# Kernel optimization log

Hardware: AMD Instinct MI355X
Metric: run time of the kernel (lower is better)

Reference implementation:

```python
import jax, jax.numpy as jnp
import numpy as np

B, S, N, D = 2048, 8, 32, 64


def setup_inputs() -> dict:
    key = jax.random.key(0)
    ks = jax.random.split(key, 13)
    s1 = 1.0 / np.sqrt(2 * D + 6)
    s2 = 1.0 / np.sqrt(D)
    s3 = 1.0 / np.sqrt(D // 2)
    return {
        "celestial_tensor": jax.random.normal(ks[0], (B, S, N, D), jnp.float32),
        "theta": jax.random.normal(ks[1], (B, N), jnp.float32),
        "phi": jax.random.normal(ks[2], (B, N), jnp.float32),
        "velocity": jax.random.normal(ks[3], (B, N), jnp.float32),
        "radius": jax.random.uniform(ks[4], (B, N), jnp.float32),
        "longitude": jax.random.normal(ks[5], (B, N), jnp.float32),
        "W1": jax.random.uniform(ks[6], (2 * D + 6, D), jnp.float32, -s1, s1),
        "b1": jax.random.uniform(ks[7], (D,), jnp.float32, -s1, s1),
        "W2": jax.random.uniform(ks[8], (D, D // 2), jnp.float32, -s2, s2),
        "b2": jax.random.uniform(ks[9], (D // 2,), jnp.float32, -s2, s2),
        "W3": jax.random.uniform(ks[10], (D // 2, 1), jnp.float32, -s3, s3),
        "b3": jax.random.uniform(ks[11], (1,), jnp.float32, -s3, s3),
        "phase_weights": jnp.ones((6,), jnp.float32),
    }


def _circ(a, b):
    # circular difference wrapped to (-pi, pi]
    d = a - b
    return jnp.arctan2(jnp.sin(d), jnp.cos(d))


def reference(celestial_tensor, theta, phi, velocity, radius, longitude,
              W1, b1, W2, b2, W3, b3, phase_weights):
    Bb, _, Nn, _ = celestial_tensor.shape
    feats = celestial_tensor[:, -1]  # [B, N, D] last timestep
    ii, jj = np.triu_indices(Nn, 1)  # static upper-tri pair indices, P pairs
    fi = feats[:, ii]  # [B, P, D]
    fj = feats[:, jj]
    td = _circ(theta[:, ii], theta[:, jj])
    pd = _circ(phi[:, ii], phi[:, jj])
    vd = velocity[:, ii] - velocity[:, jj]
    rr = radius[:, ii] / (radius[:, jj] + 1e-8)
    ld = _circ(longitude[:, ii], longitude[:, jj])
    pr = jnp.cos(td) * jnp.cos(pd)  # phase_relationship
    scal = jnp.stack([td, pd, vd, rr, ld, pr], axis=-1)  # [B, P, 6]
    x = jnp.concatenate([fi, fj, scal], axis=-1)  # [B, P, 2D+6]
    h = jax.nn.gelu(x @ W1 + b1, approximate=False)
    h = jax.nn.gelu(h @ W2 + b2, approximate=False)
    edge = jax.nn.sigmoid((h @ W3 + b3)[..., 0])  # [B, P]
    pf = jnp.stack([jnp.abs(td), jnp.abs(pd), jnp.abs(vd),
                    jnp.abs(rr - 1.0), jnp.abs(ld), jnp.abs(pr)], axis=-1)
    gate = jax.nn.sigmoid(jnp.sum(pf * phase_weights, axis=-1))
    fe = edge * gate  # [B, P]
    adj = jnp.zeros((Bb, Nn, Nn), dtype=fe.dtype)
    adj = adj.at[:, ii, jj].set(fe).at[:, jj, ii].set(fe)
    return adj
```

## Files before the change

### kernel.cpp

```cpp
#include <hip/hip_runtime.h>
#include <hip/hip_bf16.h>
#include <math.h>

#define SS 8
#define NN 32
#define DD 64
#define NP 496
#define LDA 68

typedef short v8s __attribute__((ext_vector_type(8)));
typedef float v4f __attribute__((ext_vector_type(4)));
typedef float f2  __attribute__((ext_vector_type(2)));

union FragU { uint4 u; v8s s; };
union Q2    { float4 q; f2 h[2]; };

static __device__ __forceinline__ f2 f2m(float a, float b) { f2 r; r.x = a; r.y = b; return r; }
static __device__ __forceinline__ f2 splat2(float s) { f2 r; r.x = s; r.y = s; return r; }
static __device__ __forceinline__ f2 pk_fma(f2 a, f2 b, f2 c) {
#if __has_builtin(__builtin_elementwise_fma)
    return __builtin_elementwise_fma(a, b, c);
#else
    return f2m(fmaf(a.x, b.x, c.x), fmaf(a.y, b.y, c.y));
#endif
}

__device__ __forceinline__ float wrap_pi(float d) {
    return fmaf(-6.28318530717958647692f, rintf(d * 0.15915494309189533577f), d);
}
__device__ __forceinline__ float sigmoid_(float x) {
    return __builtin_amdgcn_rcpf(1.0f + __expf(-x));
}
__device__ __forceinline__ f2 gelu2(f2 xin) {
    f2 z = xin * splat2(0.70710678118654752440f);
#if __has_builtin(__builtin_elementwise_max)
    f2 az = __builtin_elementwise_max(z, -z);
#else
    f2 az = f2m(fabsf(z.x), fabsf(z.y));
#endif
    f2 d = pk_fma(splat2(0.078108f), az, splat2(0.000972f));
    d = pk_fma(d, az, splat2(0.230389f));
    d = pk_fma(d, az, splat2(0.278393f));
    d = pk_fma(d, az, splat2(1.0f));
    f2 t = f2m(__builtin_amdgcn_rcpf(d.x), __builtin_amdgcn_rcpf(d.y));
    f2 t2 = t * t;
    f2 r = pk_fma(-t2, t2, splat2(1.0f));
    unsigned int rx = __float_as_uint(r.x) | (__float_as_uint(z.x) & 0x80000000u);
    unsigned int ry = __float_as_uint(r.y) | (__float_as_uint(z.y) & 0x80000000u);
    f2 er = f2m(__uint_as_float(rx), __uint_as_float(ry));
    return xin * pk_fma(er, splat2(0.5f), splat2(0.5f));
}
__device__ __forceinline__ unsigned int pack_bf16_rne(float x0, float x1) {
    union { __hip_bfloat162 h2; unsigned int u; } cv;
    float2 f; f.x = x0; f.y = x1;
    cv.h2 = __float22bfloat162_rn(f);
    return cv.u;
}
__device__ __forceinline__ float row_reduce16(float x) {
    int v;
    v = __builtin_amdgcn_update_dpp(0, __float_as_int(x), 0x128, 0xf, 0xf, false);
    x += __int_as_float(v);
    v = __builtin_amdgcn_update_dpp(0, __float_as_int(x), 0x124, 0xf, 0xf, false);
    x += __int_as_float(v);
    v = __builtin_amdgcn_update_dpp(0, __float_as_int(x), 0x122, 0xf, 0xf, false);
    x += __int_as_float(v);
    v = __builtin_amdgcn_update_dpp(0, __float_as_int(x), 0x121, 0xf, 0xf, false);
    x += __int_as_float(v);
    return x;
}
__device__ __forceinline__ uint4 build_w2_frag(const float* __restrict__ W2,
                                               int kb, int col) {
    uint4 pk;
    pk.x = pack_bf16_rne(W2[(kb + 0) * 32 + col], W2[(kb + 1) * 32 + col]);
    pk.y = pack_bf16_rne(W2[(kb + 2) * 32 + col], W2[(kb + 3) * 32 + col]);
    pk.z = pack_bf16_rne(W2[(kb + 4) * 32 + col], W2[(kb + 5) * 32 + col]);
    pk.w = pack_bf16_rne(W2[(kb + 6) * 32 + col], W2[(kb + 7) * 32 + col]);
    return pk;
}

__global__ __launch_bounds__(256, 2) void edge_kernel(
    const float* __restrict__ cel,
    const float* __restrict__ theta,
    const float* __restrict__ phi,
    const float* __restrict__ vel,
    const float* __restrict__ rad,
    const float* __restrict__ lon,
    const float* __restrict__ W1,
    const float* __restrict__ b1,
    const float* __restrict__ W2,
    const float* __restrict__ b2,
    const float* __restrict__ W3,
    const float* __restrict__ b3,
    const float* __restrict__ pw,
    float* __restrict__ out)
{
    __shared__ __align__(16) float sAi[NN * LDA];
    __shared__ __align__(16) float sBj[NN * LDA];
    __shared__ __align__(16) float sW1s[6 * 64];
    __shared__ float sScal[6][512];
    __shared__ float sGate[512];
    __shared__ float sTh[NN], sPh[NN], sVe[NN], sRa[NN], sLo[NN];
    __shared__ unsigned char sI[512], sJ[512];
    __shared__ float sAdj[1024];

    const int b = blockIdx.x;
    const int t = threadIdx.x;
    const int ml = t & 15;
    const int ql = (t >> 4) & 3;
    const int wv = t >> 6;
    const int kA = ql * 8;

    FragU f00, f01, f10, f11;
    f00.u = build_w2_frag(W2, 0 * 32 + kA, 0 * 16 + ml);
    f01.u = build_w2_frag(W2, 1 * 32 + kA, 0 * 16 + ml);
    f10.u = build_w2_frag(W2, 0 * 32 + kA, 1 * 16 + ml);
    f11.u = build_w2_frag(W2, 1 * 32 + kA, 1 * 16 + ml);
    const float b2v0 = b2[ml], b2v1 = b2[16 + ml];
    const float w3v0 = W3[ml], w3v1 = W3[16 + ml];
    const float b3s  = b3[0];

    if (t < NN) {
        sTh[t] = theta[b * NN + t];
        sPh[t] = phi[b * NN + t];
        sVe[t] = vel[b * NN + t];
        sRa[t] = rad[b * NN + t];
        sLo[t] = lon[b * NN + t];
    }
    if (t < 31) {
        int off = t * 31 - (t * (t - 1)) / 2;
        for (int j = t + 1; j < 32; ++j) {
            sI[off] = (unsigned char)t;
            sJ[off] = (unsigned char)j;
            ++off;
        }
    }
    for (int idx = t; idx < 1024; idx += 256) sAdj[idx] = 0.0f;
    for (int idx = t; idx < 384; idx += 256) sW1s[idx] = W1[128 * 64 + idx];
    __syncthreads();

    for (int p = t; p < NP; p += 256) {
        const int i = sI[p], j = sJ[p];
        const float td = wrap_pi(sTh[i] - sTh[j]);
        const float pd = wrap_pi(sPh[i] - sPh[j]);
        const float vd = sVe[i] - sVe[j];
        const float rr = sRa[i] * __builtin_amdgcn_rcpf(sRa[j] + 1e-8f);
        const float ld = wrap_pi(sLo[i] - sLo[j]);
        const float pr = __cosf(td) * __cosf(pd);
        sScal[0][p] = td; sScal[1][p] = pd; sScal[2][p] = vd;
        sScal[3][p] = rr; sScal[4][p] = ld; sScal[5][p] = pr;
        const float pf = fabsf(td) * pw[0] + fabsf(pd) * pw[1]
                       + fabsf(vd) * pw[2] + fabsf(rr - 1.0f) * pw[3]
                       + fabsf(ld) * pw[4] + fabsf(pr) * pw[5];
        sGate[p] = sigmoid_(pf);
    }

    {
        const int col = t & 63;
        const int w   = __builtin_amdgcn_readfirstlane(t >> 6);
        const float* fbase = cel + ((size_t)b * SS + (SS - 1)) * (NN * DD);
        f2 accA[8], accB[8];
        #pragma unroll
        for (int m = 0; m < 8; ++m) { accA[m] = splat2(0.0f); accB[m] = splat2(0.0f); }
        for (int k4 = 0; k4 < 64; k4 += 4) {
            const f2 wa01 = f2m(W1[(k4 + 0) * 64 + col], W1[(k4 + 1) * 64 + col]);
            const f2 wa23 = f2m(W1[(k4 + 2) * 64 + col], W1[(k4 + 3) * 64 + col]);
            const f2 wb01 = f2m(W1[(k4 + 64) * 64 + col], W1[(k4 + 65) * 64 + col]);
            const f2 wb23 = f2m(W1[(k4 + 66) * 64 + col], W1[(k4 + 67) * 64 + col]);
            #pragma unroll
            for (int m = 0; m < 8; ++m) {
                const float4 fv = *(const float4*)&fbase[(w + 4 * m) * 64 + k4];
                accA[m] = pk_fma(f2m(fv.x, fv.y), wa01, accA[m]);
                accA[m] = pk_fma(f2m(fv.z, fv.w), wa23, accA[m]);
                accB[m] = pk_fma(f2m(fv.x, fv.y), wb01, accB[m]);
                accB[m] = pk_fma(f2m(fv.z, fv.w), wb23, accB[m]);
            }
        }
        const float b1c = b1[col];
        #pragma unroll
        for (int m = 0; m < 8; ++m) {
            sAi[(w + 4 * m) * LDA + col] = accA[m].x + accA[m].y + b1c;
            sBj[(w + 4 * m) * LDA + col] = accB[m].x + accB[m].y;
        }
    }
    __syncthreads();

    #pragma clang loop unroll(disable)
    for (int r = 0; r < 8; ++r) {
        const int mtl = r * 4 + wv;
        if (mtl >= 31) break;
        const int p = mtl * 16 + ml;
        const int i = sI[p], j = sJ[p];
        float sc[6];
        #pragma unroll
        for (int s = 0; s < 6; ++s) sc[s] = sScal[s][p];
        const float* Ar = &sAi[i * LDA];
        const float* Br = &sBj[j * LDA];

        FragU fa0, fa1;
        {
            Q2 P0, P1, Q0, Q1;
            P0.q = *(const float4*)(Ar + kA);
            P1.q = *(const float4*)(Ar + kA + 4);
            Q0.q = *(const float4*)(Br + kA);
            Q1.q = *(const float4*)(Br + kA + 4);
            f2 v[4] = {P0.h[0] + Q0.h[0], P0.h[1] + Q0.h[1],
                       P1.h[0] + Q1.h[0], P1.h[1] + Q1.h[1]};
            #pragma unroll
            for (int s = 0; s < 6; ++s) {
                const f2 scs = splat2(sc[s]);
                Q2 W0, W1v;
                W0.q  = *(const float4*)&sW1s[s * 64 + kA];
                W1v.q = *(const float4*)&sW1s[s * 64 + kA + 4];
                v[0] = pk_fma(scs, W0.h[0],  v[0]);
                v[1] = pk_fma(scs, W0.h[1],  v[1]);
                v[2] = pk_fma(scs, W1v.h[0], v[2]);
                v[3] = pk_fma(scs, W1v.h[1], v[3]);
            }
            #pragma unroll
            for (int c = 0; c < 4; ++c) v[c] = gelu2(v[c]);
            fa0.u.x = pack_bf16_rne(v[0].x, v[0].y);
            fa0.u.y = pack_bf16_rne(v[1].x, v[1].y);
            fa0.u.z = pack_bf16_rne(v[2].x, v[2].y);
            fa0.u.w = pack_bf16_rne(v[3].x, v[3].y);
        }
        {
            Q2 P2, P3, Q2v, Q3;
            P2.q  = *(const float4*)(Ar + 32 + kA);
            P3.q  = *(const float4*)(Ar + 36 + kA);
            Q2v.q = *(const float4*)(Br + 32 + kA);
            Q3.q  = *(const float4*)(Br + 36 + kA);
            f2 y[4] = {P2.h[0] + Q2v.h[0], P2.h[1] + Q2v.h[1],
                       P3.h[0] + Q3.h[0],  P3.h[1] + Q3.h[1]};
            #pragma unroll
            for (int s = 0; s < 6; ++s) {
                const f2 scs = splat2(sc[s]);
                Q2 W0, W1v;
                W0.q  = *(const float4*)&sW1s[s * 64 + 32 + kA];
                W1v.q = *(const float4*)&sW1s[s * 64 + 36 + kA];
                y[0] = pk_fma(scs, W0.h[0],  y[0]);
                y[1] = pk_fma(scs, W0.h[1],  y[1]);
                y[2] = pk_fma(scs, W1v.h[0], y[2]);
                y[3] = pk_fma(scs, W1v.h[1], y[3]);
            }
            #pragma unroll
            for (int c = 0; c < 4; ++c) y[c] = gelu2(y[c]);
            fa1.u.x = pack_bf16_rne(y[0].x, y[0].y);
            fa1.u.y = pack_bf16_rne(y[1].x, y[1].y);
            fa1.u.z = pack_bf16_rne(y[2].x, y[2].y);
            fa1.u.w = pack_bf16_rne(y[3].x, y[3].y);
        }

        v4f acc0 = {b2v0, b2v0, b2v0, b2v0};
        v4f acc1 = {b2v1, b2v1, b2v1, b2v1};
        acc0 = __builtin_amdgcn_mfma_f32_16x16x32_bf16(fa0.s, f00.s, acc0, 0, 0, 0);
        acc0 = __builtin_amdgcn_mfma_f32_16x16x32_bf16(fa1.s, f01.s, acc0, 0, 0, 0);
        acc1 = __builtin_amdgcn_mfma_f32_16x16x32_bf16(fa0.s, f10.s, acc1, 0, 0, 0);
        acc1 = __builtin_amdgcn_mfma_f32_16x16x32_bf16(fa1.s, f11.s, acc1, 0, 0, 0);

        float cres[4];
        #pragma unroll
        for (int rr = 0; rr < 4; ++rr) {
            const f2 g = gelu2(f2m(acc0[rr], acc1[rr]));
            cres[rr] = row_reduce16(fmaf(g.y, w3v1, g.x * w3v0));
        }
        const int rsel = ml & 3;
        const float cs = (rsel & 2) ? ((rsel & 1) ? cres[3] : cres[2])
                                    : ((rsel & 1) ? cres[1] : cres[0]);
        const int pe = mtl * 16 + ql * 4 + rsel;
        const float fe = sigmoid_(cs + b3s) * sGate[pe];
        if (ml < 4) {
            const int pi = sI[pe], pj = sJ[pe];
            sAdj[pi * 32 + pj] = fe;
            sAdj[pj * 32 + pi] = fe;
        }
    }
    __syncthreads();

    float* dst = out + (size_t)b * 1024;
    for (int idx = t; idx < 1024; idx += 256) dst[idx] = sAdj[idx];
}

extern "C" void kernel_launch(void* const* d_in, const int* in_sizes, int n_in,
                              void* d_out, int out_size, void* d_ws, size_t ws_size,
                              hipStream_t stream) {
    const float* cel   = (const float*)d_in[0];
    const float* theta = (const float*)d_in[1];
    const float* phi   = (const float*)d_in[2];
    const float* vel   = (const float*)d_in[3];
    const float* rad   = (const float*)d_in[4];
    const float* lon   = (const float*)d_in[5];
    const float* W1    = (const float*)d_in[6];
    const float* b1    = (const float*)d_in[7];
    const float* W2    = (const float*)d_in[8];
    const float* b2    = (const float*)d_in[9];
    const float* W3    = (const float*)d_in[10];
    const float* b3    = (const float*)d_in[11];
    const float* pw    = (const float*)d_in[12];
    float* out = (float*)d_out;

    const int B = in_sizes[1] / NN;
    edge_kernel<<<B, 256, 0, stream>>>(cel, theta, phi, vel, rad, lon,
                                       W1, b1, W2, b2, W3, b3, pw, out);
}
```

Measured before the change: 256.9 us.

## Pack pair scalars as bf16, hoist W1 scalar weights, simplify GELU tail

Rewrites gelu2 to use |x| directly, which drops the sign-bit splicing and one multiply. The six per-pair scalars are stored in shared memory as three packed bf16 words instead of six floats, and the per-node theta/phi/etc. arrays are no longer staged in LDS but read straight from global memory. The scalar rows of W1 are hoisted into registers once, outside the main loop, instead of being reloaded from LDS on every iteration. These changes cut LDS traffic and ALU work. In exchange, the scalar features lose precision when rounded to bf16, and register pressure rises by 48 floats.

```diff
diff --git a/kernel.cpp b/kernel.cpp
--- a/kernel.cpp
+++ b/kernel.cpp
@@ -31,24 +31,23 @@
 __device__ __forceinline__ float sigmoid_(float x) {
     return __builtin_amdgcn_rcpf(1.0f + __expf(-x));
 }
-__device__ __forceinline__ f2 gelu2(f2 xin) {
-    f2 z = xin * splat2(0.70710678118654752440f);
+__device__ __forceinline__ f2 gelu2(f2 x) {
 #if __has_builtin(__builtin_elementwise_max)
-    f2 az = __builtin_elementwise_max(z, -z);
+    f2 ax = __builtin_elementwise_max(x, -x);
 #else
-    f2 az = f2m(fabsf(z.x), fabsf(z.y));
+    f2 ax = f2m(fabsf(x.x), fabsf(x.y));
 #endif
+    f2 az = ax * splat2(0.70710678118654752440f);
     f2 d = pk_fma(splat2(0.078108f), az, splat2(0.000972f));
     d = pk_fma(d, az, splat2(0.230389f));
     d = pk_fma(d, az, splat2(0.278393f));
     d = pk_fma(d, az, splat2(1.0f));
     f2 t = f2m(__builtin_amdgcn_rcpf(d.x), __builtin_amdgcn_rcpf(d.y));
     f2 t2 = t * t;
-    f2 r = pk_fma(-t2, t2, splat2(1.0f));
-    unsigned int rx = __float_as_uint(r.x) | (__float_as_uint(z.x) & 0x80000000u);
-    unsigned int ry = __float_as_uint(r.y) | (__float_as_uint(z.y) & 0x80000000u);
-    f2 er = f2m(__uint_as_float(rx), __uint_as_float(ry));
-    return xin * pk_fma(er, splat2(0.5f), splat2(0.5f));
+    f2 a = ax * splat2(0.5f);
+    f2 base = pk_fma(x, splat2(0.5f), a);
+    f2 u = a * t2;
+    return pk_fma(-u, t2, base);
 }
 __device__ __forceinline__ unsigned int pack_bf16_rne(float x0, float x1) {
     union { __hip_bfloat162 h2; unsigned int u; } cv;
@@ -56,6 +55,8 @@
     cv.h2 = __float22bfloat162_rn(f);
     return cv.u;
 }
+__device__ __forceinline__ float bf_lo(unsigned int u) { return __uint_as_float(u << 16); }
+__device__ __forceinline__ float bf_hi(unsigned int u) { return __uint_as_float(u & 0xffff0000u); }
 __device__ __forceinline__ float row_reduce16(float x) {
     int v;
     v = __builtin_amdgcn_update_dpp(0, __float_as_int(x), 0x128, 0xf, 0xf, false);
@@ -97,11 +98,10 @@
     __shared__ __align__(16) float sAi[NN * LDA];
     __shared__ __align__(16) float sBj[NN * LDA];
     __shared__ __align__(16) float sW1s[6 * 64];
-    __shared__ float sScal[6][512];
-    __shared__ float sGate[512];
-    __shared__ float sTh[NN], sPh[NN], sVe[NN], sRa[NN], sLo[NN];
-    __shared__ unsigned char sI[512], sJ[512];
     __shared__ float sAdj[1024];
+    __shared__ unsigned int sScalPk[3][NP];
+    __shared__ float sGate[NP];
+    __shared__ unsigned char sI[NP], sJ[NP];
 
     const int b = blockIdx.x;
     const int t = threadIdx.x;
@@ -119,13 +119,6 @@
     const float w3v0 = W3[ml], w3v1 = W3[16 + ml];
     const float b3s  = b3[0];
 
-    if (t < NN) {
-        sTh[t] = theta[b * NN + t];
-        sPh[t] = phi[b * NN + t];
-        sVe[t] = vel[b * NN + t];
-        sRa[t] = rad[b * NN + t];
-        sLo[t] = lon[b * NN + t];
-    }
     if (t < 31) {
         int off = t * 31 - (t * (t - 1)) / 2;
         for (int j = t + 1; j < 32; ++j) {
@@ -140,14 +133,15 @@
 
     for (int p = t; p < NP; p += 256) {
         const int i = sI[p], j = sJ[p];
-        const float td = wrap_pi(sTh[i] - sTh[j]);
-        const float pd = wrap_pi(sPh[i] - sPh[j]);
-        const float vd = sVe[i] - sVe[j];
-        const float rr = sRa[i] * __builtin_amdgcn_rcpf(sRa[j] + 1e-8f);
-        const float ld = wrap_pi(sLo[i] - sLo[j]);
+        const float td = wrap_pi(theta[b * NN + i] - theta[b * NN + j]);
+        const float pd = wrap_pi(phi[b * NN + i] - phi[b * NN + j]);
+        const float vd = vel[b * NN + i] - vel[b * NN + j];
+        const float rr = rad[b * NN + i] * __builtin_amdgcn_rcpf(rad[b * NN + j] + 1e-8f);
+        const float ld = wrap_pi(lon[b * NN + i] - lon[b * NN + j]);
         const float pr = __cosf(td) * __cosf(pd);
-        sScal[0][p] = td; sScal[1][p] = pd; sScal[2][p] = vd;
-        sScal[3][p] = rr; sScal[4][p] = ld; sScal[5][p] = pr;
+        sScalPk[0][p] = pack_bf16_rne(td, pd);
+        sScalPk[1][p] = pack_bf16_rne(vd, rr);
+        sScalPk[2][p] = pack_bf16_rne(ld, pr);
         const float pf = fabsf(td) * pw[0] + fabsf(pd) * pw[1]
                        + fabsf(vd) * pw[2] + fabsf(rr - 1.0f) * pw[3]
                        + fabsf(ld) * pw[4] + fabsf(pr) * pw[5];
@@ -184,15 +178,26 @@
     }
     __syncthreads();
 
+    f2 w1f[6][4];
+    #pragma unroll
+    for (int s = 0; s < 6; ++s) {
+        Q2 u0, u1;
+        u0.q = *(const float4*)&sW1s[s * 64 + kA];
+        u1.q = *(const float4*)&sW1s[s * 64 + kA + 4];
+        w1f[s][0] = u0.h[0]; w1f[s][1] = u0.h[1];
+        w1f[s][2] = u1.h[0]; w1f[s][3] = u1.h[1];
+    }
+
     #pragma clang loop unroll(disable)
     for (int r = 0; r < 8; ++r) {
         const int mtl = r * 4 + wv;
         if (mtl >= 31) break;
         const int p = mtl * 16 + ml;
         const int i = sI[p], j = sJ[p];
-        float sc[6];
-        #pragma unroll
-        for (int s = 0; s < 6; ++s) sc[s] = sScal[s][p];
+        const unsigned int u0 = sScalPk[0][p];
+        const unsigned int u1 = sScalPk[1][p];
+        const unsigned int u2 = sScalPk[2][p];
+        float sc[6] = {bf_lo(u0), bf_hi(u0), bf_lo(u1), bf_hi(u1), bf_lo(u2), bf_hi(u2)};
         const float* Ar = &sAi[i * LDA];
         const float* Br = &sBj[j * LDA];
 
@@ -208,13 +213,9 @@
             #pragma unroll
             for (int s = 0; s < 6; ++s) {
                 const f2 scs = splat2(sc[s]);
-                Q2 W0, W1v;
-                W0.q  = *(const float4*)&sW1s[s * 64 + kA];
-                W1v.q = *(const float4*)&sW1s[s * 64 + kA + 4];
-                v[0] = pk_fma(scs, W0.h[0],  v[0]);
-                v[1] = pk_fma(scs, W0.h[1],  v[1]);
-                v[2] = pk_fma(scs, W1v.h[0], v[2]);
-                v[3] = pk_fma(scs, W1v.h[1], v[3]);
+                #pragma unroll
+                for (int c = 0; c < 4; ++c)
+                    v[c] = pk_fma(scs, w1f[s][c], v[c]);
             }
             #pragma unroll
             for (int c = 0; c < 4; ++c) v[c] = gelu2(v[c]);
```

Result: no change. 256.9 us (+0.0%).
